# Kernel tuning notes

Hardware: AMD Instinct MI355X
Metric: run time of the kernel (lower is better)

Reference implementation:

```python
import jax, jax.numpy as jnp
import numpy as np

N_ATOMS = 100000
N_EDGES = 1600000
N_GRAPHS = 64
N_BASIS = 128
N_FILTERS = 128
N_RBF = 32
N_INTER = 6
CUTOFF = 10.0
LOG2 = float(np.log(2.0))


def ssp(x):
    # shifted softplus
    return jax.nn.softplus(x) - LOG2


def setup_inputs() -> dict:
    key = jax.random.key(0)
    ks = jax.random.split(key, 24)
    s = 0.05
    inp = {
        "z": jax.random.randint(ks[0], (N_ATOMS,), 0, 100),
        "z_res": jax.random.randint(ks[1], (N_ATOMS,), 0, 100),
        "pos": jax.random.normal(ks[2], (N_ATOMS, 3), jnp.float32) * 5.0,
        "idx_i": jax.random.randint(ks[3], (N_EDGES,), 0, N_ATOMS),
        "idx_j": jax.random.randint(ks[4], (N_EDGES,), 0, N_ATOMS),
        "edge_attr": jax.random.randint(ks[5], (N_EDGES,), 0, 4),
        "batch": jnp.sort(jax.random.randint(ks[6], (N_ATOMS,), 0, N_GRAPHS)),
        "ele_emb": jax.random.normal(ks[7], (100, N_BASIS), jnp.float32) * s,
        "res_emb": jax.random.normal(ks[8], (100, N_BASIS), jnp.float32) * s,
        "edge_emb": jax.random.normal(ks[9], (4, N_RBF), jnp.float32) * s,
        "in2f_W": jax.random.normal(ks[10], (N_INTER, N_BASIS, N_FILTERS), jnp.float32) * s,
        "filt_W1": jax.random.normal(ks[11], (N_INTER, N_RBF, N_FILTERS), jnp.float32) * s,
        "filt_b1": jnp.zeros((N_INTER, N_FILTERS), jnp.float32),
        "filt_W2": jax.random.normal(ks[12], (N_INTER, N_FILTERS, N_FILTERS), jnp.float32) * s,
        "filt_b2": jnp.zeros((N_INTER, N_FILTERS), jnp.float32),
        "f2out_W1": jax.random.normal(ks[13], (N_INTER, N_FILTERS, N_BASIS), jnp.float32) * s,
        "f2out_b1": jnp.zeros((N_INTER, N_BASIS), jnp.float32),
        "f2out_W2": jax.random.normal(ks[14], (N_INTER, N_BASIS, N_BASIS), jnp.float32) * s,
        "f2out_b2": jnp.zeros((N_INTER, N_BASIS), jnp.float32),
        "head_W1": jax.random.normal(ks[15], (N_BASIS, N_BASIS), jnp.float32) * s,
        "head_b1": jnp.zeros((N_BASIS,), jnp.float32),
        "head_W2": jax.random.normal(ks[16], (N_BASIS, 1), jnp.float32) * s,
    }
    return inp


def _forward(z, z_res, pos, idx_i, idx_j, edge_attr, batch,
             ele_emb, res_emb, edge_emb,
             in2f_W, filt_W1, filt_b1, filt_W2, filt_b2,
             f2out_W1, f2out_b1, f2out_W2, f2out_b2,
             head_W1, head_b1, head_W2):
    # distances per edge
    r_ij = pos[idx_i] - pos[idx_j]                       # [E,3]
    d_ij = jnp.linalg.norm(r_ij, axis=1)                 # [E]

    # Gaussian RBF expansion: offsets linspace(0, cutoff, n_rbf)
    offsets = jnp.linspace(0.0, CUTOFF, N_RBF)
    width = offsets[1] - offsets[0]
    coeff = -0.5 / (width * width)
    f_ij = jnp.exp(coeff * (d_ij[:, None] - offsets[None, :]) ** 2)  # [E,R]
    f_ij = f_ij + edge_emb[edge_attr]

    # cosine cutoff
    rcut_ij = 0.5 * (jnp.cos(d_ij * jnp.pi / CUTOFF) + 1.0) * (d_ij < CUTOFF)

    # atom embeddings
    x = ele_emb[z] + res_emb[z_res]                      # [N,B]

    for i in range(N_INTER):
        xf = x @ in2f_W[i]                               # [N,F]
        Wij = ssp(f_ij @ filt_W1[i] + filt_b1[i]) @ filt_W2[i] + filt_b2[i]
        Wij = Wij * rcut_ij[:, None]                     # [E,F]
        x_ij = xf[idx_j] * Wij                           # gather + multiply
        agg = jax.ops.segment_sum(x_ij, idx_i, num_segments=N_ATOMS)  # scatter_add
        v = ssp(agg @ f2out_W1[i] + f2out_b1[i]) @ f2out_W2[i] + f2out_b2[i]
        x = x + v

    # L2 normalize then head
    h = x / jnp.maximum(jnp.linalg.norm(x, axis=-1, keepdims=True), 1e-12)
    h = jax.nn.silu(h) @ head_W1 + head_b1
    h = jax.nn.silu(h) @ head_W2                         # [N,1]
    new_y = jax.ops.segment_sum(h, batch, num_segments=N_GRAPHS)  # [G,1]
    return new_y.squeeze(-1)


def reference(z, z_res, pos, idx_i, idx_j, edge_attr, batch,
              ele_emb, res_emb, edge_emb,
              in2f_W, filt_W1, filt_b1, filt_W2, filt_b2,
              f2out_W1, f2out_b1, f2out_W2, f2out_b2,
              head_W1, head_b1, head_W2):
    return _forward(z, z_res, pos, idx_i, idx_j, edge_attr, batch,
                    ele_emb, res_emb, edge_emb,
                    in2f_W, filt_W1, filt_b1, filt_W2, filt_b2,
                    f2out_W1, f2out_b1, f2out_W2, f2out_b2,
                    head_W1, head_b1, head_W2)
```

## Files before the change

### kernel.cpp

```cpp
#include <hip/hip_runtime.h>
#include <hip/hip_bf16.h>
#include <math.h>

#define NB 128
#define NR 32
#define EPAD 40
#define HPAD 136
#define SCB 256


static constexpr float CUTOFF_F    = 10.0f;
static constexpr float RBF_STEP    = 10.0f / 31.0f;
static constexpr float RBF_COEFF   = -4.805f;
static constexpr float LOG2_F      = 0.69314718055994531f;
static constexpr float PI_OVER_CUT = 0.314159265358979f;

typedef __attribute__((ext_vector_type(8))) short bf16x8;
typedef __attribute__((ext_vector_type(2))) short bf16x2;
typedef __attribute__((ext_vector_type(4))) float f32x4;

__device__ __forceinline__ short f2bs(float x) {
    __hip_bfloat16 h = __float2bfloat16(x);
    return *reinterpret_cast<short*>(&h);
}
__device__ __forceinline__ float bs2f(unsigned short u) {
    unsigned int v = ((unsigned int)u) << 16;
    return __uint_as_float(v);
}
__device__ __forceinline__ float ssp_f(float v) {
    return fmaxf(v, 0.0f) + __logf(1.0f + __expf(-fabsf(v))) - LOG2_F;
}
__device__ __forceinline__ float silu_f(float v) {
    return v / (1.0f + __expf(-v));
}

__device__ __forceinline__ void atomic_pk_add_bf16(short* addr, float lo, float hi) {
#if __has_builtin(__builtin_amdgcn_global_atomic_fadd_v2bf16)
    typedef bf16x2 __attribute__((address_space(1))) *gptr;
    bf16x2 v;
    v[0] = f2bs(lo);
    v[1] = f2bs(hi);
    __builtin_amdgcn_global_atomic_fadd_v2bf16((gptr)(unsigned long long)addr, v);
#else
    unsigned int* w = (unsigned int*)addr;
    unsigned int old = *w, assumed;
    do {
        assumed = old;
        float fl = bs2f((unsigned short)(assumed & 0xffff)) + lo;
        float fh = bs2f((unsigned short)(assumed >> 16)) + hi;
        unsigned int nv = ((unsigned int)(unsigned short)f2bs(fh) << 16) |
                          (unsigned short)f2bs(fl);
        old = atomicCAS(w, assumed, nv);
    } while (old != assumed);
#endif
}

__device__ __forceinline__ void flush_pk(short* aggrow, const float* accum, int col) {
    bool even = ((col & 1) == 0);
#pragma unroll
    for (int q = 0; q < 4; q++) {
        float a = accum[2 * q], b = accum[2 * q + 1];
        float pa = __shfl_xor(a, 1);
        float pb = __shfl_xor(b, 1);
        int nbase = even ? (2 * q) * 16 + col : (2 * q + 1) * 16 + (col - 1);
        float lo = even ? a : pb;
        float hi = even ? pa : b;
        atomic_pk_add_bf16(aggrow + nbase, lo, hi);
    }
}

__global__ void transpose_cvt(const float* __restrict__ src, short* __restrict__ dst,
                              int R, int C, int total) {
    int t = blockIdx.x * blockDim.x + threadIdx.x;
    if (t >= total) return;
    int rc = R * C;
    int b = t / rc;
    int rem = t - b * rc;
    int c = rem / R;
    int r = rem - c * R;
    dst[t] = f2bs(src[(size_t)b * rc + (size_t)r * C + c]);
}

__global__ void edge_prep4(const float* __restrict__ pos,
                           const int* __restrict__ idx_i,
                           const int* __restrict__ idx_j,
                           float* __restrict__ d_ij,
                           int* __restrict__ hist,
                           int E) {
    int b0 = blockIdx.x * 1024 + threadIdx.x;
    int ia[4], ib[4];
    bool val[4];
#pragma unroll
    for (int k = 0; k < 4; k++) {
        int e = b0 + k * 256;
        val[k] = (e < E);
        ia[k] = val[k] ? idx_i[e] : 0;
        ib[k] = val[k] ? idx_j[e] : 0;
    }
    float ax[4], ay[4], az[4], bx[4], by[4], bz[4];
#pragma unroll
    for (int k = 0; k < 4; k++) {
        const float* pa = pos + ia[k] * 3;
        ax[k] = pa[0]; ay[k] = pa[1]; az[k] = pa[2];
    }
#pragma unroll
    for (int k = 0; k < 4; k++) {
        const float* pb = pos + ib[k] * 3;
        bx[k] = pb[0]; by[k] = pb[1]; bz[k] = pb[2];
    }
#pragma unroll
    for (int k = 0; k < 4; k++) {
        if (!val[k]) continue;
        float dx = ax[k] - bx[k], dy = ay[k] - by[k], dz = az[k] - bz[k];
        float d = sqrtf(dx * dx + dy * dy + dz * dz);
        d_ij[b0 + k * 256] = d;
        if (d < CUTOFF_F) atomicAdd(&hist[ia[k]], 1);
    }
}

__global__ __launch_bounds__(256) void scan_reduce(const int* __restrict__ hist,
                                                   int* __restrict__ partial, int N) {
    __shared__ int red[256];
    int b = blockIdx.x;
    int chunk = (N + SCB - 1) / SCB;
    int lo = b * chunk;
    int hi = min(lo + chunk, N);
    int s = 0;
    for (int i = lo + threadIdx.x; i < hi; i += 256) s += hist[i];
    red[threadIdx.x] = s;
    __syncthreads();
    for (int d = 128; d > 0; d >>= 1) {
        if (threadIdx.x < d) red[threadIdx.x] += red[threadIdx.x + d];
        __syncthreads();
    }
    if (threadIdx.x == 0) partial[b] = red[0];
}

__global__ __launch_bounds__(256) void scan_partials(int* __restrict__ partial) {
    __shared__ int sm[SCB];
    int t = threadIdx.x;
    sm[t] = partial[t];
    __syncthreads();
    for (int d = 1; d < SCB; d <<= 1) {
        int v = (t >= d) ? sm[t - d] : 0;
        __syncthreads();
        sm[t] += v;
        __syncthreads();
    }
    partial[t] = (t == 0) ? 0 : sm[t - 1];
}

__global__ __launch_bounds__(256) void scan_expand(const int* __restrict__ hist,
                                                   const int* __restrict__ partial,
                                                   int* __restrict__ cursor, int N) {
    __shared__ int tsum[256];
    int b = blockIdx.x;
    int chunk = (N + SCB - 1) / SCB;
    int lo = b * chunk;
    int hi = min(lo + chunk, N);
    int sub = (chunk + 255) / 256;
    int tlo = lo + threadIdx.x * sub;
    int thi = min(tlo + sub, hi);
    int s = 0;
    for (int i = tlo; i < thi; i++) s += hist[i];
    int t = threadIdx.x;
    tsum[t] = s;
    __syncthreads();
    for (int d = 1; d < 256; d <<= 1) {
        int v = (t >= d) ? tsum[t - d] : 0;
        __syncthreads();
        tsum[t] += v;
        __syncthreads();
    }
    int run = partial[b] + ((t == 0) ? 0 : tsum[t - 1]);
    for (int i = tlo; i < thi; i++) {
        cursor[i] = run;
        run += hist[i];
    }
}

__global__ void scatter_sorted4(const float* __restrict__ d_ij,
                                const int* __restrict__ idx_i,
                                const int* __restrict__ idx_j,
                                const int* __restrict__ edge_attr,
                                int* __restrict__ cursor,
                                float4* __restrict__ edata,
                                int* __restrict__ sIarr, int E) {
    int b0 = blockIdx.x * 1024 + threadIdx.x;
    float d[4]; int ii[4], jj[4], at[4]; bool act[4];
#pragma unroll
    for (int k = 0; k < 4; k++) {
        int e = b0 + k * 256;
        bool v = (e < E);
        d[k] = v ? d_ij[e] : 1e9f;
        act[k] = (d[k] < CUTOFF_F);
        ii[k] = act[k] ? idx_i[e] : 0;
        jj[k] = act[k] ? idx_j[e] : 0;
        at[k] = act[k] ? edge_attr[e] : 0;
    }
    int p[4];
#pragma unroll
    for (int k = 0; k < 4; k++)
        if (act[k]) p[k] = atomicAdd(&cursor[ii[k]], 1);
#pragma unroll
    for (int k = 0; k < 4; k++) {
        if (!act[k]) continue;
        float4 v;
        v.x = d[k];
        v.y = 0.5f * (__cosf(d[k] * PI_OVER_CUT) + 1.0f);
        v.z = __int_as_float(jj[k]);
        v.w = __int_as_float(at[k]);
        edata[p[k]] = v;
        sIarr[p[k]] = ii[k];
    }
}

__global__ void atom_embed(const int* __restrict__ z,
                           const int* __restrict__ z_res,
                           const float* __restrict__ ele_emb,
                           const float* __restrict__ res_emb,
                           float* __restrict__ x, int N) {
    int t = blockIdx.x * blockDim.x + threadIdx.x;
    if (t >= N * NB) return;
    int n = t >> 7, c = t & 127;
    x[t] = ele_emb[z[n] * NB + c] + res_emb[z_res[n] * NB + c];
}

__global__ __launch_bounds__(256, 4) void node_in2f_mfma(
    const float* __restrict__ x, const short* __restrict__ WT,
    short* __restrict__ xf, int N) {
    __shared__ __align__(16) short XA[64 * HPAD];
    int a0 = blockIdx.x * 64;
    int t = threadIdx.x;
#pragma unroll
    for (int c = 0; c < 4; c++) {
        int chunk = t + c * 256;
        int row = chunk >> 4;
        int col = (chunk & 15) * 8;
        short v[8];
        if (a0 + row < N) {
            const float* src = x + (size_t)(a0 + row) * NB + col;
            float4 f0 = *(const float4*)src;
            float4 f1 = *(const float4*)(src + 4);
            v[0] = f2bs(f0.x); v[1] = f2bs(f0.y); v[2] = f2bs(f0.z); v[3] = f2bs(f0.w);
            v[4] = f2bs(f1.x); v[5] = f2bs(f1.y); v[6] = f2bs(f1.z); v[7] = f2bs(f1.w);
        } else {
#pragma unroll
            for (int j = 0; j < 8; j++) v[j] = 0;
        }
        *(bf16x8*)&XA[row * HPAD + col] = *(bf16x8*)v;
    }
    __syncthreads();

    int wid = t >> 6, lane = t & 63;
    int quad = lane >> 4, col = lane & 15;
    int mrow = wid * 16 + col;

    f32x4 acc[8] = {};
#pragma unroll
    for (int kt = 0; kt < 4; kt++) {
        bf16x8 a = *(bf16x8*)&XA[mrow * HPAD + kt * 32 + quad * 8];
#pragma unroll
        for (int nt = 0; nt < 8; nt++) {
            bf16x8 b = *(const bf16x8*)&WT[(nt * 16 + col) * NB + kt * 32 + quad * 8];
            acc[nt] = __builtin_amdgcn_mfma_f32_16x16x32_bf16(a, b, acc[nt], 0, 0, 0);
        }
    }
#pragma unroll
    for (int nt = 0; nt < 8; nt++) {
        int cst = col * 8 + nt;
#pragma unroll
        for (int r = 0; r < 4; r++) {
            int m = wid * 16 + quad * 4 + r;
            if (a0 + m < N) xf[(size_t)(a0 + m) * NB + cst] = f2bs(acc[nt][r]);
        }
    }
}

__global__ __launch_bounds__(128, 1) void node_fused_mfma(
    short* __restrict__ agg,
    const short* __restrict__ W1T, const float* __restrict__ b1,
    const short* __restrict__ W2T, const float* __restrict__ b2,
    const short* __restrict__ WnT,
    float* __restrict__ x, short* __restrict__ xf, int N) {
    __shared__ __align__(16) short XA[64 * HPAD];
    __shared__ __align__(16) short H[64 * HPAD];
    int a0 = blockIdx.x * 64;
    int t = threadIdx.x;
    int wid = t >> 6, lane = t & 63;
    int quad = lane >> 4, col = lane & 15;

#pragma unroll
    for (int c = 0; c < 8; c++) {
        int chunk = lane + c * 64;
        int row = wid * 32 + (chunk >> 4);
        int colb = (chunk & 15) * 8;
        bf16x8 v = {0, 0, 0, 0, 0, 0, 0, 0};
        if (a0 + row < N) {
            short* src = agg + (size_t)(a0 + row) * NB + colb;
            v = *(const bf16x8*)src;
            *(bf16x8*)src = (bf16x8){0, 0, 0, 0, 0, 0, 0, 0};
        }
        *(bf16x8*)&XA[row * HPAD + colb] = v;
    }
    asm volatile("s_waitcnt lgkmcnt(0)" ::: "memory");
    __builtin_amdgcn_sched_barrier(0);

    {
        f32x4 acc[2][8] = {};
#pragma unroll
        for (int kt = 0; kt < 4; kt++) {
            bf16x8 bf[8];
#pragma unroll
            for (int nt = 0; nt < 8; nt++)
                bf[nt] = *(const bf16x8*)&W1T[(nt * 16 + col) * NB + kt * 32 + quad * 8];
#pragma unroll
            for (int s = 0; s < 2; s++) {
                bf16x8 a = *(bf16x8*)&XA[(wid * 32 + s * 16 + col) * HPAD + kt * 32 + quad * 8];
#pragma unroll
                for (int nt = 0; nt < 8; nt++)
                    acc[s][nt] = __builtin_amdgcn_mfma_f32_16x16x32_bf16(a, bf[nt], acc[s][nt], 0, 0, 0);
            }
        }
#pragma unroll
        for (int s = 0; s < 2; s++) {
#pragma unroll
            for (int nt = 0; nt < 8; nt++) {
                int n = nt * 16 + col;
                float bias = b1[n];
#pragma unroll
                for (int r = 0; r < 4; r++) {
                    int m = wid * 32 + s * 16 + quad * 4 + r;
                    H[m * HPAD + n] = f2bs(ssp_f(acc[s][nt][r] + bias));
                }
            }
        }
    }
    asm volatile("s_waitcnt lgkmcnt(0)" ::: "memory");
    __builtin_amdgcn_sched_barrier(0);

    {
        f32x4 acc[2][8] = {};
#pragma unroll
        for (int kt = 0; kt < 4; kt++) {
            bf16x8 bf[8];
#pragma unroll
            for (int nt = 0; nt < 8; nt++)
                bf[nt] = *(const bf16x8*)&W2T[(nt * 16 + col) * NB + kt * 32 + quad * 8];
#pragma unroll
            for (int s = 0; s < 2; s++) {
                bf16x8 a = *(bf16x8*)&H[(wid * 32 + s * 16 + col) * HPAD + kt * 32 + quad * 8];
#pragma unroll
                for (int nt = 0; nt < 8; nt++)
                    acc[s][nt] = __builtin_amdgcn_mfma_f32_16x16x32_bf16(a, bf[nt], acc[s][nt], 0, 0, 0);
            }
        }
#pragma unroll
        for (int s = 0; s < 2; s++) {
#pragma unroll
            for (int nt = 0; nt < 8; nt++) {
                int n = nt * 16 + col;
                float bias = b2[n];
#pragma unroll
                for (int r = 0; r < 4; r++) {
                    int m = wid * 32 + s * 16 + quad * 4 + r;
                    float xn = 0.0f;
                    if (a0 + m < N) {
                        size_t o = (size_t)(a0 + m) * NB + n;
                        xn = x[o] + acc[s][nt][r] + bias;
                        x[o] = xn;
                    }
                    XA[m * HPAD + n] = f2bs(xn);
                }
            }
        }
    }
    asm volatile("s_waitcnt lgkmcnt(0)" ::: "memory");
    __builtin_amdgcn_sched_barrier(0);

    {
        f32x4 acc[2][8] = {};
#pragma unroll
        for (int kt = 0; kt < 4; kt++) {
            bf16x8 bf[8];
#pragma unroll
            for (int nt = 0; nt < 8; nt++)
                bf[nt] = *(const bf16x8*)&WnT[(nt * 16 + col) * NB + kt * 32 + quad * 8];
#pragma unroll
            for (int s = 0; s < 2; s++) {
                bf16x8 a = *(bf16x8*)&XA[(wid * 32 + s * 16 + col) * HPAD + kt * 32 + quad * 8];
#pragma unroll
                for (int nt = 0; nt < 8; nt++)
                    acc[s][nt] = __builtin_amdgcn_mfma_f32_16x16x32_bf16(a, bf[nt], acc[s][nt], 0, 0, 0);
            }
        }
#pragma unroll
        for (int s = 0; s < 2; s++) {
#pragma unroll
            for (int nt = 0; nt < 8; nt++) {
                int cst = col * 8 + nt;
#pragma unroll
                for (int r = 0; r < 4; r++) {
                    int m = wid * 32 + s * 16 + quad * 4 + r;
                    if (a0 + m < N) xf[(size_t)(a0 + m) * NB + cst] = f2bs(acc[s][nt][r]);
                }
            }
        }
    }
}

__global__ __launch_bounds__(256, 4) void node_out_head_mfma(
    const short* __restrict__ agg,
    const short* __restrict__ W1T, const float* __restrict__ b1,
    const short* __restrict__ W2T, const float* __restrict__ b2,
    const float* __restrict__ x, const int* __restrict__ batch,
    const short* __restrict__ hW1T, const float* __restrict__ hb1,
    const float* __restrict__ hW2,
    float* __restrict__ out, int N) {
    __shared__ __align__(16) short XA[64 * HPAD];
    __shared__ __align__(16) short H[64 * HPAD];
    __shared__ int sbat[64];
    __shared__ float rowval[64];
    int a0 = blockIdx.x * 64;
    int t = threadIdx.x;

    if (t < 64) sbat[t] = (a0 + t < N) ? batch[a0 + t] : -1;
#pragma unroll
    for (int c = 0; c < 4; c++) {
        int chunk = t + c * 256;
        int row = chunk >> 4;
        int col = (chunk & 15) * 8;
        bf16x8 v = {0, 0, 0, 0, 0, 0, 0, 0};
        if (a0 + row < N) v = *(const bf16x8*)&agg[(size_t)(a0 + row) * NB + col];
        *(bf16x8*)&XA[row * HPAD + col] = v;
    }
    __syncthreads();

    int wid = t >> 6, lane = t & 63;
    int quad = lane >> 4, col = lane & 15;
    int mrow = wid * 16 + col;

    {
        f32x4 acc[8] = {};
#pragma unroll
        for (int kt = 0; kt < 4; kt++) {
            bf16x8 a = *(bf16x8*)&XA[mrow * HPAD + kt * 32 + quad * 8];
#pragma unroll
            for (int nt = 0; nt < 8; nt++) {
                bf16x8 b = *(const bf16x8*)&W1T[(nt * 16 + col) * NB + kt * 32 + quad * 8];
                acc[nt] = __builtin_amdgcn_mfma_f32_16x16x32_bf16(a, b, acc[nt], 0, 0, 0);
            }
        }
#pragma unroll
        for (int nt = 0; nt < 8; nt++) {
            int n = nt * 16 + col;
            float bias = b1[n];
#pragma unroll
            for (int r = 0; r < 4; r++) {
                int m = wid * 16 + quad * 4 + r;
                H[m * HPAD + n] = f2bs(ssp_f(acc[nt][r] + bias));
            }
        }
    }
    __syncthreads();

    float xnv[8][4];
    float ssq[4] = {0.f, 0.f, 0.f, 0.f};
    {
        f32x4 acc[8] = {};
#pragma unroll
        for (int kt = 0; kt < 4; kt++) {
            bf16x8 a = *(bf16x8*)&H[mrow * HPAD + kt * 32 + quad * 8];
#pragma unroll
            for (int nt = 0; nt < 8; nt++) {
                bf16x8 b = *(const bf16x8*)&W2T[(nt * 16 + col) * NB + kt * 32 + quad * 8];
                acc[nt] = __builtin_amdgcn_mfma_f32_16x16x32_bf16(a, b, acc[nt], 0, 0, 0);
            }
        }
#pragma unroll
        for (int nt = 0; nt < 8; nt++) {
            int n = nt * 16 + col;
            float bias = b2[n];
#pragma unroll
            for (int r = 0; r < 4; r++) {
                int m = wid * 16 + quad * 4 + r;
                float xn = 0.0f;
                if (a0 + m < N) xn = x[(size_t)(a0 + m) * NB + n] + acc[nt][r] + bias;
                xnv[nt][r] = xn;
                ssq[r] += xn * xn;
            }
        }
    }
#pragma unroll
    for (int r = 0; r < 4; r++) {
#pragma unroll
        for (int m = 1; m < 16; m <<= 1) ssq[r] += __shfl_xor(ssq[r], m);
    }
    float inv[4];
#pragma unroll
    for (int r = 0; r < 4; r++) inv[r] = 1.0f / fmaxf(sqrtf(ssq[r]), 1e-12f);
    __syncthreads();
#pragma unroll
    for (int nt = 0; nt < 8; nt++) {
        int n = nt * 16 + col;
#pragma unroll
        for (int r = 0; r < 4; r++) {
            int m = wid * 16 + quad * 4 + r;
            XA[m * HPAD + n] = f2bs(silu_f(xnv[nt][r] * inv[r]));
        }
    }
    __syncthreads();

    f32x4 acc[8] = {};
#pragma unroll
    for (int kt = 0; kt < 4; kt++) {
        bf16x8 a = *(bf16x8*)&XA[mrow * HPAD + kt * 32 + quad * 8];
#pragma unroll
        for (int nt = 0; nt < 8; nt++) {
            bf16x8 b = *(const bf16x8*)&hW1T[(nt * 16 + col) * NB + kt * 32 + quad * 8];
            acc[nt] = __builtin_amdgcn_mfma_f32_16x16x32_bf16(a, b, acc[nt], 0, 0, 0);
        }
    }
    float partial[4] = {0.f, 0.f, 0.f, 0.f};
#pragma unroll
    for (int nt = 0; nt < 8; nt++) {
        int n = nt * 16 + col;
        float bias = hb1[n];
        float w2 = hW2[n];
#pragma unroll
        for (int r = 0; r < 4; r++) partial[r] += silu_f(acc[nt][r] + bias) * w2;
    }
#pragma unroll
    for (int r = 0; r < 4; r++) {
#pragma unroll
        for (int d = 1; d < 16; d <<= 1) partial[r] += __shfl_xor(partial[r], d);
    }
    if (col == 0) {
#pragma unroll
        for (int r = 0; r < 4; r++) rowval[wid * 16 + quad * 4 + r] = partial[r];
    }
    __syncthreads();

    if (t < 64) {
        int b = sbat[t];
        bool headf = (b >= 0) && (t == 0 || sbat[t - 1] != b);
        if (headf) {
            float s = 0.0f;
            int rr = t;
            while (rr < 64 && sbat[rr] == b) { s += rowval[rr]; rr++; }
            atomicAdd(&out[b], s);
        }
    }
}

__global__ __launch_bounds__(256, 3) void edge_fused_mfma(
    const float4* __restrict__ edata, const int* __restrict__ sIarr,
    const int* __restrict__ rowend, int natoms,
    const float* __restrict__ edge_emb,
    const short* __restrict__ W1T, const float* __restrict__ b1,
    const short* __restrict__ W2T, const float* __restrict__ b2,
    const short* __restrict__ xf, short* __restrict__ agg) {
    __shared__ __align__(16) short fA[128 * EPAD];
    __shared__ __align__(16) short H[128 * HPAD];

    int t = threadIdx.x;
    int wid = t >> 6, lane = t & 63;
    int quad = lane >> 4, col = lane & 15;
    int base = blockIdx.x * 128;
    int wbase = base + wid * 32;
    int el32 = lane & 31;

    float4 ed = edata[wbase + el32];
    int sIv0 = sIarr[wbase + el32];
    int cnt = rowend[natoms - 1];
    if (base >= cnt) return;

    bool act = (wbase + el32) < cnt;
    float dv  = act ? ed.x : 1e9f;
    float rcv = act ? ed.y : 0.0f;
    int   jjv = act ? __float_as_int(ed.z) : 0;
    int   atv = act ? __float_as_int(ed.w) : 0;
    int   iiv = act ? sIv0 : 0;

    {
        int elA = lane >> 1;
        int r0 = (lane & 1) * 16;
        float d  = __shfl(dv, elA);
        int   at = __shfl(atv, elA);
        const float* em = edge_emb + at * NR + r0;
        short v[16];
#pragma unroll
        for (int j = 0; j < 16; j++) {
            float off = (float)(r0 + j) * RBF_STEP;
            float dd = d - off;
            v[j] = f2bs(__expf(RBF_COEFF * dd * dd) + em[j]);
        }
        short* dst = &fA[(wid * 32 + elA) * EPAD + r0];
        *(bf16x8*)dst = *(bf16x8*)v;
        *(bf16x8*)(dst + 8) = *(bf16x8*)(v + 8);
    }

    bf16x8 xv[2][4];
    const unsigned short* xg = (const unsigned short*)xf;
#pragma unroll
    for (int s = 0; s < 2; s++) {
#pragma unroll
        for (int r = 0; r < 4; r++) {
            int jj = __shfl(jjv, s * 16 + quad * 4 + r);
            xv[s][r] = *(const bf16x8*)&xg[(size_t)jj * NB + col * 8];
        }
    }

    asm volatile("s_waitcnt lgkmcnt(0)" ::: "memory");
    __builtin_amdgcn_sched_barrier(0);

    {
        bf16x8 b1f[8];
#pragma unroll
        for (int nt = 0; nt < 8; nt++)
            b1f[nt] = *(const bf16x8*)&W1T[(nt * 16 + col) * NR + quad * 8];
#pragma unroll
        for (int s = 0; s < 2; s++) {
            bf16x8 a1 = *(bf16x8*)&fA[(wid * 32 + s * 16 + col) * EPAD + quad * 8];
            f32x4 acc[8];
#pragma unroll
            for (int nt = 0; nt < 8; nt++)
                acc[nt] = __builtin_amdgcn_mfma_f32_16x16x32_bf16(a1, b1f[nt], (f32x4){0.f, 0.f, 0.f, 0.f}, 0, 0, 0);
#pragma unroll
            for (int nt = 0; nt < 8; nt++) {
                int n = nt * 16 + col;
                float bias = b1[n];
#pragma unroll
                for (int r = 0; r < 4; r++) {
                    int m = wid * 32 + s * 16 + quad * 4 + r;
                    H[m * HPAD + n] = f2bs(ssp_f(acc[nt][r] + bias));
                }
            }
        }
    }

    asm volatile("s_waitcnt lgkmcnt(0)" ::: "memory");
    __builtin_amdgcn_sched_barrier(0);

    f32x4 acc2[2][8] = {};
#pragma unroll
    for (int kt = 0; kt < 4; kt++) {
        bf16x8 b2f[8];
#pragma unroll
        for (int nt = 0; nt < 8; nt++)
            b2f[nt] = *(const bf16x8*)&W2T[(nt * 16 + col) * NB + kt * 32 + quad * 8];
#pragma unroll
        for (int s = 0; s < 2; s++) {
            bf16x8 a = *(bf16x8*)&H[(wid * 32 + s * 16 + col) * HPAD + kt * 32 + quad * 8];
#pragma unroll
            for (int nt = 0; nt < 8; nt++)
                acc2[s][nt] = __builtin_amdgcn_mfma_f32_16x16x32_bf16(a, b2f[nt], acc2[s][nt], 0, 0, 0);
        }
    }

    float b2v[8];
#pragma unroll
    for (int nt = 0; nt < 8; nt++) b2v[nt] = b2[nt * 16 + col];

#pragma unroll
    for (int s = 0; s < 2; s++) {
        int e0l = s * 16 + quad * 4;
        int cur = __shfl(iiv, e0l);
        float accum[8] = {0.f, 0.f, 0.f, 0.f, 0.f, 0.f, 0.f, 0.f};
#pragma unroll
        for (int r = 0; r < 4; r++) {
            int ii = __shfl(iiv, e0l + r);
            float rc = __shfl(rcv, e0l + r);
            if (ii != cur) {
                flush_pk(agg + (size_t)cur * NB, accum, col);
#pragma unroll
                for (int nt = 0; nt < 8; nt++) accum[nt] = 0.f;
                cur = ii;
            }
#pragma unroll
            for (int nt = 0; nt < 8; nt++) {
                float w = (acc2[s][nt][r] + b2v[nt]) * rc;
                accum[nt] = fmaf(w, bs2f((unsigned short)xv[s][r][nt]), accum[nt]);
            }
        }
        flush_pk(agg + (size_t)cur * NB, accum, col);
    }
}

extern "C" void kernel_launch(void* const* d_in, const int* in_sizes, int n_in,
                              void* d_out, int out_size, void* d_ws, size_t ws_size,
                              hipStream_t stream) {
    const int*   z        = (const int*)d_in[0];
    const int*   z_res    = (const int*)d_in[1];
    const float* pos      = (const float*)d_in[2];
    const int*   idx_i    = (const int*)d_in[3];
    const int*   idx_j    = (const int*)d_in[4];
    const int*   edge_attr= (const int*)d_in[5];
    const int*   batch    = (const int*)d_in[6];
    const float* ele_emb  = (const float*)d_in[7];
    const float* res_emb  = (const float*)d_in[8];
    const float* edge_emb = (const float*)d_in[9];
    const float* in2f_W   = (const float*)d_in[10];
    const float* filt_W1  = (const float*)d_in[11];
    const float* filt_b1  = (const float*)d_in[12];
    const float* filt_W2  = (const float*)d_in[13];
    const float* filt_b2  = (const float*)d_in[14];
    const float* f2out_W1 = (const float*)d_in[15];
    const float* f2out_b1 = (const float*)d_in[16];
    const float* f2out_W2 = (const float*)d_in[17];
    const float* f2out_b2 = (const float*)d_in[18];
    const float* head_W1  = (const float*)d_in[19];
    const float* head_b1  = (const float*)d_in[20];
    const float* head_W2  = (const float*)d_in[21];

    const int N = in_sizes[0];
    const int E = in_sizes[3];

    char* p = (char*)d_ws;
    size_t off = 0;
    auto carve = [&](size_t bytes) -> void* {
        void* q = p + off;
        off = (off + bytes + 255) & ~(size_t)255;
        return q;
    };
    float*  d_d      = (float*)carve((size_t)E * 4);
    float4* edata    = (float4*)carve((size_t)E * 16);
    int*    sIarr    = (int*)carve((size_t)E * 4);
    int*    hist     = (int*)carve((size_t)N * 4);
    int*    cursor   = (int*)carve((size_t)N * 4);
    int*    partial  = (int*)carve((size_t)SCB * 4);
    float*  x_buf    = (float*)carve((size_t)N * NB * 4);
    short*  xf_buf   = (short*)carve((size_t)N * NB * 2);
    short*  agg      = (short*)carve((size_t)N * NB * 2);
    short*  in2f_WT  = (short*)carve((size_t)6 * NB * NB * 2);
    short*  fW1T     = (short*)carve((size_t)6 * NR * NB * 2);
    short*  fW2T     = (short*)carve((size_t)6 * NB * NB * 2);
    short*  oW1T     = (short*)carve((size_t)6 * NB * NB * 2);
    short*  oW2T     = (short*)carve((size_t)6 * NB * NB * 2);
    short*  hW1T     = (short*)carve((size_t)NB * NB * 2);
    (void)ws_size;

    {
        int tot = 6 * NB * NB;
        transpose_cvt<<<(tot + 255) / 256, 256, 0, stream>>>(in2f_W, in2f_WT, NB, NB, tot);
        transpose_cvt<<<(tot + 255) / 256, 256, 0, stream>>>(filt_W2, fW2T, NB, NB, tot);
        transpose_cvt<<<(tot + 255) / 256, 256, 0, stream>>>(f2out_W1, oW1T, NB, NB, tot);
        transpose_cvt<<<(tot + 255) / 256, 256, 0, stream>>>(f2out_W2, oW2T, NB, NB, tot);
        int tot1 = 6 * NR * NB;
        transpose_cvt<<<(tot1 + 255) / 256, 256, 0, stream>>>(filt_W1, fW1T, NR, NB, tot1);
        int tot2 = NB * NB;
        transpose_cvt<<<(tot2 + 255) / 256, 256, 0, stream>>>(head_W1, hW1T, NB, NB, tot2);
    }

    hipMemsetAsync(hist, 0, (size_t)N * 4, stream);
    int nblk_e4 = (E + 1023) / 1024;
    edge_prep4<<<nblk_e4, 256, 0, stream>>>(pos, idx_i, idx_j, d_d, hist, E);
    scan_reduce<<<SCB, 256, 0, stream>>>(hist, partial, N);
    scan_partials<<<1, SCB, 0, stream>>>(partial);
    scan_expand<<<SCB, 256, 0, stream>>>(hist, partial, cursor, N);
    scatter_sorted4<<<nblk_e4, 256, 0, stream>>>(d_d, idx_i, idx_j, edge_attr,
                                                 cursor, edata, sIarr, E);

    atom_embed<<<(N * NB + 255) / 256, 256, 0, stream>>>(z, z_res, ele_emb, res_emb, x_buf, N);

    int nblk_atom64 = (N + 63) / 64;
    int nblk_edge = (E + 127) / 128;

    node_in2f_mfma<<<nblk_atom64, 256, 0, stream>>>(x_buf, in2f_WT, xf_buf, N);
    hipMemsetAsync(d_out, 0, (size_t)out_size * sizeof(float), stream);
    hipMemsetAsync(agg, 0, (size_t)N * NB * 2, stream);
    for (int i = 0; i < 6; i++) {
        edge_fused_mfma<<<nblk_edge, 256, 0, stream>>>(
            edata, sIarr, cursor, N, edge_emb,
            fW1T + (size_t)i * NR * NB, filt_b1 + (size_t)i * NB,
            fW2T + (size_t)i * NB * NB, filt_b2 + (size_t)i * NB,
            xf_buf, agg);
        if (i < 5) {
            node_fused_mfma<<<nblk_atom64, 128, 0, stream>>>(
                agg, oW1T + (size_t)i * NB * NB, f2out_b1 + (size_t)i * NB,
                oW2T + (size_t)i * NB * NB, f2out_b2 + (size_t)i * NB,
                in2f_WT + (size_t)(i + 1) * NB * NB,
                x_buf, xf_buf, N);
        } else {
            node_out_head_mfma<<<nblk_atom64, 256, 0, stream>>>(
                agg, oW1T + (size_t)i * NB * NB, f2out_b1 + (size_t)i * NB,
                oW2T + (size_t)i * NB * NB, f2out_b2 + (size_t)i * NB,
                x_buf, batch, hW1T, head_b1, head_W2,
                (float*)d_out, N);
        }
    }
}
```

Baseline: 1.875 ms.

## Process 64 edges per wave in edge kernel with 128-thread blocks

The edge kernel now runs two waves per block, each handling 64 edges instead of 32, so each wave loads the W1/W2 B-fragments once and reuses them across four 16-row M tiles. The gather of xf rows for the second half of the edges is issued after the second GEMM to limit register pressure. The goal is to halve per-edge weight fragment loads and amortize fixed per-wave overhead. In exchange, the acc2 accumulators double, which raises VGPR use and may lower occupancy. Dropping the minimum-blocks launch bound also lets the compiler use more registers.

```diff
diff --git a/kernel.cpp b/kernel.cpp
--- a/kernel.cpp
+++ b/kernel.cpp
@@ -553,7 +553,7 @@
     }
 }
 
-__global__ __launch_bounds__(256, 3) void edge_fused_mfma(
+__global__ __launch_bounds__(128) void edge_fused_mfma(
     const float4* __restrict__ edata, const int* __restrict__ sIarr,
     const int* __restrict__ rowend, int natoms,
     const float* __restrict__ edge_emb,
@@ -567,47 +567,49 @@
     int wid = t >> 6, lane = t & 63;
     int quad = lane >> 4, col = lane & 15;
     int base = blockIdx.x * 128;
-    int wbase = base + wid * 32;
-    int el32 = lane & 31;
-
-    float4 ed = edata[wbase + el32];
-    int sIv0 = sIarr[wbase + el32];
+    int wbase = base + wid * 64;
+
+    float4 ed = edata[wbase + lane];
+    int sIv0 = sIarr[wbase + lane];
     int cnt = rowend[natoms - 1];
     if (base >= cnt) return;
 
-    bool act = (wbase + el32) < cnt;
+    bool act = (wbase + lane) < cnt;
     float dv  = act ? ed.x : 1e9f;
     float rcv = act ? ed.y : 0.0f;
     int   jjv = act ? __float_as_int(ed.z) : 0;
     int   atv = act ? __float_as_int(ed.w) : 0;
     int   iiv = act ? sIv0 : 0;
 
+    const unsigned short* xg = (const unsigned short*)xf;
+
     {
-        int elA = lane >> 1;
-        int r0 = (lane & 1) * 16;
-        float d  = __shfl(dv, elA);
-        int   at = __shfl(atv, elA);
-        const float* em = edge_emb + at * NR + r0;
-        short v[16];
-#pragma unroll
-        for (int j = 0; j < 16; j++) {
-            float off = (float)(r0 + j) * RBF_STEP;
-            float dd = d - off;
-            v[j] = f2bs(__expf(RBF_COEFF * dd * dd) + em[j]);
-        }
-        short* dst = &fA[(wid * 32 + elA) * EPAD + r0];
-        *(bf16x8*)dst = *(bf16x8*)v;
-        *(bf16x8*)(dst + 8) = *(bf16x8*)(v + 8);
-    }
-
-    bf16x8 xv[2][4];
-    const unsigned short* xg = (const unsigned short*)xf;
+#pragma unroll
+        for (int c = 0; c < 4; c++) {
+            int chunk = lane + c * 64;
+            int row = chunk >> 2;
+            int r0 = (chunk & 3) * 8;
+            float d  = __shfl(dv, row);
+            int   at = __shfl(atv, row);
+            const float* em = edge_emb + at * NR + r0;
+            short v[8];
+#pragma unroll
+            for (int j = 0; j < 8; j++) {
+                float off = (float)(r0 + j) * RBF_STEP;
+                float dd = d - off;
+                v[j] = f2bs(__expf(RBF_COEFF * dd * dd) + em[j]);
+            }
+            *(bf16x8*)&fA[(wid * 64 + row) * EPAD + r0] = *(bf16x8*)v;
+        }
+    }
+
+    bf16x8 xv01[2][4];
 #pragma unroll
     for (int s = 0; s < 2; s++) {
 #pragma unroll
         for (int r = 0; r < 4; r++) {
             int jj = __shfl(jjv, s * 16 + quad * 4 + r);
-            xv[s][r] = *(const bf16x8*)&xg[(size_t)jj * NB + col * 8];
+            xv01[s][r] = *(const bf16x8*)&xg[(size_t)jj * NB + col * 8];
         }
     }
 
@@ -620,8 +622,8 @@
         for (int nt = 0; nt < 8; nt++)
             b1f[nt] = *(const bf16x8*)&W1T[(nt * 16 + col) * NR + quad * 8];
 #pragma unroll
-        for (int s = 0; s < 2; s++) {
-            bf16x8 a1 = *(bf16x8*)&fA[(wid * 32 + s * 16 + col) * EPAD + quad * 8];
+        for (int s = 0; s < 4; s++) {
+            bf16x8 a1 = *(bf16x8*)&fA[(wid * 64 + s * 16 + col) * EPAD + quad * 8];
             f32x4 acc[8];
 #pragma unroll
             for (int nt = 0; nt < 8; nt++)
@@ -632,7 +634,7 @@
                 float bias = b1[n];
 #pragma unroll
                 for (int r = 0; r < 4; r++) {
-                    int m = wid * 32 + s * 16 + quad * 4 + r;
+                    int m = wid * 64 + s * 16 + quad * 4 + r;
                     H[m * HPAD + n] = f2bs(ssp_f(acc[nt][r] + bias));
                 }
             }
@@ -642,7 +644,7 @@
     asm volatile("s_waitcnt lgkmcnt(0)" ::: "memory");
     __builtin_amdgcn_sched_barrier(0);
 
-    f32x4 acc2[2][8] = {};
+    f32x4 acc2[4][8] = {};
 #pragma unroll
     for (int kt = 0; kt < 4; kt++) {
         bf16x8 b2f[8];
@@ -650,20 +652,30 @@
         for (int nt = 0; nt < 8; nt++)
             b2f[nt] = *(const bf16x8*)&W2T[(nt * 16 + col) * NB + kt * 32 + quad * 8];
 #pragma unroll
-        for (int s = 0; s < 2; s++) {
-            bf16x8 a = *(bf16x8*)&H[(wid * 32 + s * 16 + col) * HPAD + kt * 32 + quad * 8];
+        for (int s = 0; s < 4; s++) {
+            bf16x8 a = *(bf16x8*)&H[(wid * 64 + s * 16 + col) * HPAD + kt * 32 + quad * 8];
 #pragma unroll
             for (int nt = 0; nt < 8; nt++)
                 acc2[s][nt] = __builtin_amdgcn_mfma_f32_16x16x32_bf16(a, b2f[nt], acc2[s][nt], 0, 0, 0);
         }
     }
 
+    bf16x8 xv23[2][4];
+#pragma unroll
+    for (int s = 0; s < 2; s++) {
+#pragma unroll
+        for (int r = 0; r < 4; r++) {
+            int jj = __shfl(jjv, (s + 2) * 16 + quad * 4 + r);
+            xv23[s][r] = *(const bf16x8*)&xg[(size_t)jj * NB + col * 8];
+        }
+    }
+
     float b2v[8];
 #pragma unroll
     for (int nt = 0; nt < 8; nt++) b2v[nt] = b2[nt * 16 + col];
 
 #pragma unroll
-    for (int s = 0; s < 2; s++) {
+    for (int s = 0; s < 4; s++) {
         int e0l = s * 16 + quad * 4;
         int cur = __shfl(iiv, e0l);
         float accum[8] = {0.f, 0.f, 0.f, 0.f, 0.f, 0.f, 0.f, 0.f};
@@ -677,10 +689,11 @@
                 for (int nt = 0; nt < 8; nt++) accum[nt] = 0.f;
                 cur = ii;
             }
+            bf16x8 xvv = (s < 2) ? xv01[s][r] : xv23[s - 2][r];
 #pragma unroll
             for (int nt = 0; nt < 8; nt++) {
                 float w = (acc2[s][nt][r] + b2v[nt]) * rc;
-                accum[nt] = fmaf(w, bs2f((unsigned short)xv[s][r][nt]), accum[nt]);
+                accum[nt] = fmaf(w, bs2f((unsigned short)xvv[nt]), accum[nt]);
             }
         }
         flush_pk(agg + (size_t)cur * NB, accum, col);
@@ -770,7 +783,7 @@
     hipMemsetAsync(d_out, 0, (size_t)out_size * sizeof(float), stream);
     hipMemsetAsync(agg, 0, (size_t)N * NB * 2, stream);
     for (int i = 0; i < 6; i++) {
-        edge_fused_mfma<<<nblk_edge, 256, 0, stream>>>(
+        edge_fused_mfma<<<nblk_edge, 128, 0, stream>>>(
             edata, sIarr, cursor, N, edge_emb,
             fW1T + (size_t)i * NR * NB, filt_b1 + (size_t)i * NB,
             fW2T + (size_t)i * NB * NB, filt_b2 + (size_t)i * NB,
```

Result: slower. 2.208 ms (+17.8%).
